# Kernel optimization log

Measured on AMD Instinct MI355X. Metric: run time of the kernel, lower is better.

## Reference

```python
import jax, jax.numpy as jnp
import numpy as np

D_MODEL = 1024
NUM_HEADS = 16
HEAD_DIM = D_MODEL // NUM_HEADS
THETA = 10000.0


def _rope(x):
    # x: [B, H, S, Dk]; interleaved even/odd rotation as in the torch module
    *_, seq_len, d_k = x.shape
    d = d_k // 2
    inv_freq = 1.0 / (THETA ** (2.0 * jnp.arange(d, dtype=jnp.float32) / d_k))
    pos = jnp.arange(seq_len, dtype=jnp.float32)
    angles = pos[:, None] * inv_freq[None, :]  # [S, d]
    cos = jnp.cos(angles)
    sin = jnp.sin(angles)
    x_even = x[..., 0::2]
    x_odd = x[..., 1::2]
    rot_even = x_even * cos - x_odd * sin
    rot_odd = x_even * sin + x_odd * cos
    return jnp.stack([rot_even, rot_odd], axis=-1).reshape(x.shape)


def setup_inputs() -> dict:
    key = jax.random.key(0)
    ks = jax.random.split(key, 5)
    B, S = 4, 2048
    x = jax.random.normal(ks[0], (B, S, D_MODEL), dtype=jnp.float32)
    q_w = jax.random.uniform(ks[1], (D_MODEL, D_MODEL), dtype=jnp.float32)
    k_w = jax.random.uniform(ks[2], (D_MODEL, D_MODEL), dtype=jnp.float32)
    v_w = jax.random.uniform(ks[3], (D_MODEL, D_MODEL), dtype=jnp.float32)
    o_w = jax.random.uniform(ks[4], (D_MODEL, D_MODEL), dtype=jnp.float32)
    return {"x": x, "q_w": q_w, "k_w": k_w, "v_w": v_w, "o_w": o_w}


def reference(x, q_w, k_w, v_w, o_w):
    B, S, _ = x.shape
    def split_heads(t):
        return t.reshape(B, S, NUM_HEADS, HEAD_DIM).transpose(0, 2, 1, 3)  # [B,H,S,Dk]
    Q = split_heads(x @ q_w.T)
    K = split_heads(x @ k_w.T)
    V = split_heads(x @ v_w.T)
    Q = _rope(Q)
    K = _rope(K)
    scale = 1.0 / jnp.sqrt(jnp.float32(HEAD_DIM))
    scores = jnp.einsum('bhqd,bhkd->bhqk', Q, K) * scale  # [B,H,S,S]
    causal = jnp.tril(jnp.ones((S, S), dtype=bool))
    scores = jnp.where(causal[None, None], scores, -jnp.inf)
    attn = jax.nn.softmax(scores, axis=-1)
    out = jnp.einsum('bhqk,bhkd->bhqd', attn, V)  # [B,H,S,Dk]
    out = out.transpose(0, 2, 1, 3).reshape(B, S, D_MODEL)
    return out @ o_w.T
```

## Files before the change

### kernel.cpp

```cpp
#include <hip/hip_runtime.h>
#include <hip/hip_bf16.h>
#include <cstdint>
#include <cstddef>

#define D_MODEL   1024
#define NUM_HEADS 16
#define HEAD_DIM  64
#define SEQ       2048
#define BATCH     4
#define BH        (BATCH*NUM_HEADS)
#define MROWS     (BATCH*SEQ)

typedef _Float16 half8  __attribute__((ext_vector_type(8)));
typedef _Float16 half4v __attribute__((ext_vector_type(4)));
typedef float    floatx4 __attribute__((ext_vector_type(4)));

__device__ inline void gld_lds16(const void* g, void* l) {
    __builtin_amdgcn_global_load_lds(
        (__attribute__((address_space(1))) void*)g,
        (__attribute__((address_space(3))) void*)l,
        16, 0, 0);
}

__global__ void rope_table(float2* __restrict__ tab) {
    const int i = blockIdx.x * blockDim.x + threadIdx.x;
    const int p = i & 31, s = i >> 5;
    const double inv = pow(10000.0, -(double)p / 32.0);
    const double ang = (double)s * inv;
    tab[i] = make_float2((float)cos(ang), (float)sin(ang));
}

__global__ void f32_to_f16_v4(const float* __restrict__ in,
                              _Float16* __restrict__ out, int n4) {
    int i = blockIdx.x * blockDim.x + threadIdx.x;
    if (i >= n4) return;
    float4 v = ((const float4*)in)[i];
    half4v o = { (_Float16)v.x, (_Float16)v.y, (_Float16)v.z, (_Float16)v.w };
    ((half4v*)out)[i] = o;
}

__global__ void f32_split_f16(const float* __restrict__ in,
                              _Float16* __restrict__ hi,
                              _Float16* __restrict__ lo, int n4) {
    int i = blockIdx.x * blockDim.x + threadIdx.x;
    if (i >= n4) return;
    float4 v = ((const float4*)in)[i];
    half4v h = { (_Float16)v.x, (_Float16)v.y, (_Float16)v.z, (_Float16)v.w };
    half4v l = { (_Float16)(v.x - (float)h.x), (_Float16)(v.y - (float)h.y),
                 (_Float16)(v.z - (float)h.z), (_Float16)(v.w - (float)h.w) };
    ((half4v*)hi)[i] = h;
    ((half4v*)lo)[i] = l;
}

template<int MODE>
__global__ __launch_bounds__(256)
void gemm_bt(const _Float16* __restrict__ A, const _Float16* __restrict__ B,
             void* __restrict__ Cout, int M, int N, int K) {
    __shared__ _Float16 As[128*32];
    __shared__ _Float16 Bs[128*32];

    const int nb = N >> 7;
    const int bx = blockIdx.x % nb;
    const int by = blockIdx.x / nb;
    const int m0 = by << 7, n0 = bx << 7;

    const int t    = threadIdx.x;
    const int w    = t >> 6;
    const int lane = t & 63;
    const int r    = lane & 15;
    const int quad = lane >> 4;
    const int wm   = (w >> 1) << 6;
    const int wn   = (w & 1) << 6;

    const int srow = lane >> 2;
    const int scol = (lane & 3) << 3;

    floatx4 acc[4][4];
    #pragma unroll
    for (int i = 0; i < 4; i++)
        #pragma unroll
        for (int j = 0; j < 4; j++)
            acc[i][j] = (floatx4){0.f, 0.f, 0.f, 0.f};

    for (int k0 = 0; k0 < K; k0 += 32) {
        __syncthreads();
        #pragma unroll
        for (int p = 0; p < 2; ++p) {
            const int rbase = p*64 + w*16;
            gld_lds16(&A[(size_t)(m0 + rbase + srow)*K + k0 + scol], &As[rbase*32]);
            gld_lds16(&B[(size_t)(n0 + rbase + srow)*K + k0 + scol], &Bs[rbase*32]);
        }
        __syncthreads();

        half8 af[4], bf[4];
        #pragma unroll
        for (int i = 0; i < 4; i++)
            af[i] = *(const half8*)&As[(wm + i*16 + r)*32 + quad*8];
        #pragma unroll
        for (int j = 0; j < 4; j++)
            bf[j] = *(const half8*)&Bs[(wn + j*16 + r)*32 + quad*8];

        #pragma unroll
        for (int i = 0; i < 4; i++)
            #pragma unroll
            for (int j = 0; j < 4; j++)
                acc[i][j] = __builtin_amdgcn_mfma_f32_16x16x32_f16(
                                af[i], bf[j], acc[i][j], 0, 0, 0);
    }

    #pragma unroll
    for (int i = 0; i < 4; i++) {
        #pragma unroll
        for (int j = 0; j < 4; j++) {
            #pragma unroll
            for (int v = 0; v < 4; v++) {
                const int m = m0 + wm + i*16 + quad*4 + v;
                const int n = n0 + wn + j*16 + r;
                const float val = acc[i][j][v];
                if (MODE == 0) {
                    ((float*)Cout)[(size_t)m*N + n] = val;
                } else {
                    const int b = m >> 11, s = m & 2047;
                    const int h = n >> 6,  d = n & 63;
                    ((_Float16*)Cout)[((((size_t)b*NUM_HEADS + h)*HEAD_DIM + d) << 11) + s]
                        = (_Float16)val;
                }
            }
        }
    }
}

__global__ __launch_bounds__(256)
void gemm_qk(const _Float16* __restrict__ Ah, const _Float16* __restrict__ Al,
             const _Float16* __restrict__ Bh, const _Float16* __restrict__ Bl,
             _Float16* __restrict__ Chi, _Float16* __restrict__ Clo,
             const float2* __restrict__ tab, int M, int N, int K) {
    __shared__ _Float16 Ash[128*32];
    __shared__ _Float16 Asl[128*32];
    __shared__ _Float16 Bsh[128*32];
    __shared__ _Float16 Bsl[128*32];

    const int nb = N >> 7;
    const int bx = blockIdx.x % nb;
    const int by = blockIdx.x / nb;
    const int m0 = by << 7, n0 = bx << 7;

    const int t    = threadIdx.x;
    const int w    = t >> 6;
    const int lane = t & 63;
    const int r    = lane & 15;
    const int quad = lane >> 4;
    const int wm   = (w >> 1) << 6;
    const int wn   = (w & 1) << 6;

    const int srow = lane >> 2;
    const int scol = (lane & 3) << 3;

    floatx4 acc[4][4];
    #pragma unroll
    for (int i = 0; i < 4; i++)
        #pragma unroll
        for (int j = 0; j < 4; j++)
            acc[i][j] = (floatx4){0.f, 0.f, 0.f, 0.f};

    for (int k0 = 0; k0 < K; k0 += 32) {
        __syncthreads();
        #pragma unroll
        for (int p = 0; p < 2; ++p) {
            const int rbase = p*64 + w*16;
            const size_t ga = (size_t)(m0 + rbase + srow)*K + k0 + scol;
            const size_t gb = (size_t)(n0 + rbase + srow)*K + k0 + scol;
            gld_lds16(&Ah[ga], &Ash[rbase*32]);
            gld_lds16(&Al[ga], &Asl[rbase*32]);
            gld_lds16(&Bh[gb], &Bsh[rbase*32]);
            gld_lds16(&Bl[gb], &Bsl[rbase*32]);
        }
        __syncthreads();

        half8 ah[4], al[4], bh[4], bl[4];
        #pragma unroll
        for (int i = 0; i < 4; i++) {
            ah[i] = *(const half8*)&Ash[(wm + i*16 + r)*32 + quad*8];
            al[i] = *(const half8*)&Asl[(wm + i*16 + r)*32 + quad*8];
        }
        #pragma unroll
        for (int j = 0; j < 4; j++) {
            bh[j] = *(const half8*)&Bsh[(wn + j*16 + r)*32 + quad*8];
            bl[j] = *(const half8*)&Bsl[(wn + j*16 + r)*32 + quad*8];
        }

        #pragma unroll
        for (int i = 0; i < 4; i++)
            #pragma unroll
            for (int j = 0; j < 4; j++) {
                acc[i][j] = __builtin_amdgcn_mfma_f32_16x16x32_f16(
                                ah[i], bh[j], acc[i][j], 0, 0, 0);
                acc[i][j] = __builtin_amdgcn_mfma_f32_16x16x32_f16(
                                ah[i], bl[j], acc[i][j], 0, 0, 0);
                acc[i][j] = __builtin_amdgcn_mfma_f32_16x16x32_f16(
                                al[i], bh[j], acc[i][j], 0, 0, 0);
            }
    }

    #pragma unroll
    for (int i = 0; i < 4; i++) {
        #pragma unroll
        for (int v = 0; v < 4; v++) {
            const int m  = m0 + wm + i*16 + quad*4 + v;
            const int b  = m >> 11;
            const int s_ = m & 2047;
            #pragma unroll
            for (int j = 0; j < 4; j++) {
                const int n = n0 + wn + j*16 + r;
                const int h = n >> 6, d = n & 63;
                const float val = acc[i][j][v];
                const float pv  = __shfl_xor(val, 1);
                const float2 cs = tab[s_*32 + (d >> 1)];
                const float res = (r & 1) ? (pv*cs.y + val*cs.x)
                                          : (val*cs.x - pv*cs.y);
                const size_t idx = ((((size_t)b*NUM_HEADS + h)*SEQ + s_) << 6) + d;
                const _Float16 hv = (_Float16)res;
                Chi[idx] = hv;
                Clo[idx] = (_Float16)(res - (float)hv);
            }
        }
    }
}

#define PSTR 72
__global__ __launch_bounds__(256)
void flash_attn(const _Float16* __restrict__ Qhi, const _Float16* __restrict__ Qlo,
                const _Float16* __restrict__ Khi, const _Float16* __restrict__ Klo,
                const _Float16* __restrict__ Vt,  _Float16* __restrict__ AO) {
    __shared__ _Float16 Ksh0[64*32];
    __shared__ _Float16 Ksh1[64*32];
    __shared__ _Float16 Ksl0[64*32];
    __shared__ _Float16 Ksl1[64*32];
    __shared__ _Float16 Vs0 [64*32];
    __shared__ _Float16 Vs1 [64*32];
    __shared__ _Float16 Pl  [4][16*PSTR];

    const int t    = threadIdx.x;
    const int w    = t >> 6;
    const int lane = t & 63;
    const int r    = lane & 15;
    const int quad = lane >> 4;

    const int bx = blockIdx.x;
    const int bh = bx & 63;
    const int qb = 31 - (bx >> 6);
    const int q0w = qb*64 + w*16;
    const int b  = bh >> 4, h = bh & 15;

    const _Float16* Qh_ = Qhi + (size_t)bh * SEQ * HEAD_DIM;
    const _Float16* Ql_ = Qlo + (size_t)bh * SEQ * HEAD_DIM;
    const _Float16* Khg = Khi + (size_t)bh * SEQ * HEAD_DIM;
    const _Float16* Klg = Klo + (size_t)bh * SEQ * HEAD_DIM;
    const _Float16* Vtg = Vt  + (size_t)bh * HEAD_DIM * SEQ;

    half8 qh[2], ql[2];
    #pragma unroll
    for (int c = 0; c < 2; ++c) {
        qh[c] = *(const half8*)&Qh_[(size_t)(q0w + r)*64 + c*32 + quad*8];
        ql[c] = *(const half8*)&Ql_[(size_t)(q0w + r)*64 + c*32 + quad*8];
    }

    floatx4 ot[4];
    #pragma unroll
    for (int dt = 0; dt < 4; ++dt) ot[dt] = (floatx4){0.f,0.f,0.f,0.f};
    float mi = -1e30f, li = 0.f;

    const int sr = lane >> 2;
    const int sc = (lane & 3) << 3;

    const int niter = qb + 1;
    for (int kt = 0; kt < niter; ++kt) {
        const int k0 = kt << 6;

        __syncthreads();
        {
            const int rb  = w << 4;
            const int row = rb + sr;
            const size_t kr = (size_t)(k0 + row)*64;
            gld_lds16(&Khg[kr +      sc], &Ksh0[rb*32]);
            gld_lds16(&Khg[kr + 32 + sc], &Ksh1[rb*32]);
            gld_lds16(&Klg[kr +      sc], &Ksl0[rb*32]);
            gld_lds16(&Klg[kr + 32 + sc], &Ksl1[rb*32]);
            const size_t vr = (size_t)row*SEQ + k0;
            gld_lds16(&Vtg[vr +      sc], &Vs0[rb*32]);
            gld_lds16(&Vtg[vr + 32 + sc], &Vs1[rb*32]);
        }
        __syncthreads();

        float s[16];
        #pragma unroll
        for (int sub = 0; sub < 4; ++sub) {
            floatx4 a = (floatx4){0.f,0.f,0.f,0.f};
            const int fr = (sub*16 + r)*32 + quad*8;
            const half8 kh0 = *(const half8*)&Ksh0[fr];
            const half8 kh1 = *(const half8*)&Ksh1[fr];
            const half8 kl0 = *(const half8*)&Ksl0[fr];
            const half8 kl1 = *(const half8*)&Ksl1[fr];
            a = __builtin_amdgcn_mfma_f32_16x16x32_f16(kh0, qh[0], a, 0, 0, 0);
            a = __builtin_amdgcn_mfma_f32_16x16x32_f16(kh1, qh[1], a, 0, 0, 0);
            a = __builtin_amdgcn_mfma_f32_16x16x32_f16(kh0, ql[0], a, 0, 0, 0);
            a = __builtin_amdgcn_mfma_f32_16x16x32_f16(kh1, ql[1], a, 0, 0, 0);
            a = __builtin_amdgcn_mfma_f32_16x16x32_f16(kl0, qh[0], a, 0, 0, 0);
            a = __builtin_amdgcn_mfma_f32_16x16x32_f16(kl1, qh[1], a, 0, 0, 0);
            #pragma unroll
            for (int v = 0; v < 4; ++v) s[sub*4 + v] = a[v] * 0.125f;
        }

        if (kt == niter - 1) {
            #pragma unroll
            for (int sub = 0; sub < 4; ++sub)
                #pragma unroll
                for (int v = 0; v < 4; ++v)
                    if (k0 + sub*16 + quad*4 + v > q0w + r)
                        s[sub*4 + v] = -1e30f;
        }

        float tm = s[0];
        #pragma unroll
        for (int i = 1; i < 16; ++i) tm = fmaxf(tm, s[i]);
        tm = fmaxf(tm, __shfl_xor(tm, 16));
        tm = fmaxf(tm, __shfl_xor(tm, 32));
        const float mn = fmaxf(mi, tm);
        const float alpha = __expf(mi - mn);
        mi = mn;
        float rs = 0.f;
        #pragma unroll
        for (int i = 0; i < 16; ++i) { s[i] = __expf(s[i] - mn); rs += s[i]; }
        rs += __shfl_xor(rs, 16);
        rs += __shfl_xor(rs, 32);
        li = li*alpha + rs;
        #pragma unroll
        for (int dt = 0; dt < 4; ++dt)
            #pragma unroll
            for (int v = 0; v < 4; ++v) ot[dt][v] *= alpha;

        #pragma unroll
        for (int sub = 0; sub < 4; ++sub) {
            half4v pk = { (_Float16)s[sub*4+0], (_Float16)s[sub*4+1],
                          (_Float16)s[sub*4+2], (_Float16)s[sub*4+3] };
            *(half4v*)&Pl[w][r*PSTR + sub*16 + quad*4] = pk;
        }

        #pragma unroll
        for (int c = 0; c < 2; ++c) {
            const half8 pf = *(const half8*)&Pl[w][r*PSTR + c*32 + quad*8];
            const _Float16* Vsc = c ? Vs1 : Vs0;
            #pragma unroll
            for (int dt = 0; dt < 4; ++dt) {
                const half8 vf = *(const half8*)&Vsc[(dt*16 + r)*32 + quad*8];
                ot[dt] = __builtin_amdgcn_mfma_f32_16x16x32_f16(vf, pf, ot[dt], 0, 0, 0);
            }
        }
    }

    const float inv = 1.0f / li;
    const int q = q0w + r;
    #pragma unroll
    for (int dt = 0; dt < 4; ++dt) {
        half4v o = { (_Float16)(ot[dt][0]*inv), (_Float16)(ot[dt][1]*inv),
                     (_Float16)(ot[dt][2]*inv), (_Float16)(ot[dt][3]*inv) };
        *(half4v*)&AO[((size_t)(b*SEQ + q))*D_MODEL + h*HEAD_DIM + dt*16 + quad*4] = o;
    }
}

extern "C" void kernel_launch(void* const* d_in, const int* in_sizes, int n_in,
                              void* d_out, int out_size, void* d_ws, size_t ws_size,
                              hipStream_t stream) {
    const float* x  = (const float*)d_in[0];
    const float* qw = (const float*)d_in[1];
    const float* kw = (const float*)d_in[2];
    const float* vw = (const float*)d_in[3];
    const float* ow = (const float*)d_in[4];
    float* out = (float*)d_out;

    _Float16* xh  = (_Float16*)d_ws;
    _Float16* xl  = xh  + (size_t)MROWS * D_MODEL;
    _Float16* qwh = xl  + (size_t)MROWS * D_MODEL;
    _Float16* qwl = qwh + (size_t)D_MODEL * D_MODEL;
    _Float16* kwh = qwl + (size_t)D_MODEL * D_MODEL;
    _Float16* kwl = kwh + (size_t)D_MODEL * D_MODEL;
    _Float16* vwh = kwl + (size_t)D_MODEL * D_MODEL;
    _Float16* owh = vwh + (size_t)D_MODEL * D_MODEL;
    _Float16* Qhi = owh + (size_t)D_MODEL * D_MODEL;
    _Float16* Qlo = Qhi + (size_t)MROWS * D_MODEL;
    _Float16* Khi = Qlo + (size_t)MROWS * D_MODEL;
    _Float16* Klo = Khi + (size_t)MROWS * D_MODEL;
    _Float16* Vt  = Klo + (size_t)MROWS * D_MODEL;
    _Float16* AO  = Vt  + (size_t)MROWS * D_MODEL;
    float2*   tab = (float2*)(AO + (size_t)MROWS * D_MODEL);

    rope_table<<<(SEQ*32)/256, 256, 0, stream>>>(tab);

    const int nx4 = MROWS * D_MODEL / 4;
    f32_split_f16<<<nx4/256, 256, 0, stream>>>(x, xh, xl, nx4);
    const int nw4 = D_MODEL * D_MODEL / 4;
    f32_split_f16<<<nw4/256, 256, 0, stream>>>(qw, qwh, qwl, nw4);
    f32_split_f16<<<nw4/256, 256, 0, stream>>>(kw, kwh, kwl, nw4);
    f32_to_f16_v4<<<nw4/256, 256, 0, stream>>>(vw, vwh, nw4);
    f32_to_f16_v4<<<nw4/256, 256, 0, stream>>>(ow, owh, nw4);

    const int gemm_grid = (MROWS/128) * (D_MODEL/128);
    gemm_qk<<<gemm_grid, 256, 0, stream>>>(xh, xl, qwh, qwl, Qhi, Qlo, tab,
                                           MROWS, D_MODEL, D_MODEL);
    gemm_qk<<<gemm_grid, 256, 0, stream>>>(xh, xl, kwh, kwl, Khi, Klo, tab,
                                           MROWS, D_MODEL, D_MODEL);
    gemm_bt<2><<<gemm_grid, 256, 0, stream>>>(xh, vwh, Vt, MROWS, D_MODEL, D_MODEL);

    flash_attn<<<BH * (SEQ/64), 256, 0, stream>>>(Qhi, Qlo, Khi, Klo, Vt, AO);

    gemm_bt<0><<<gemm_grid, 256, 0, stream>>>(AO, owh, out, MROWS, D_MODEL, D_MODEL);
}
```

Measured before the change: 393.4 us.

## Fuse QKV projections into one launch and widen flash-attention blocks to 128 queries

Merges the four weight-conversion launches into one kernel, and merges the Q, K and V projection GEMMs into a single launch whose grid selects the weight matrix per block. Flash attention now runs 512-thread blocks covering 128 queries with 8 waves sharing each K/V tile, so every tile is loaded once for twice as many queries. Waves whose rows lie entirely before a tile skip its compute, and causal masking is applied per wave. This cuts launch count and K/V reload traffic, at the cost of uneven per-wave work inside a block and a larger block that may lower occupancy.

```diff
diff --git a/kernel.cpp b/kernel.cpp
--- a/kernel.cpp
+++ b/kernel.cpp
@@ -28,15 +28,6 @@
     const double inv = pow(10000.0, -(double)p / 32.0);
     const double ang = (double)s * inv;
     tab[i] = make_float2((float)cos(ang), (float)sin(ang));
-}
-
-__global__ void f32_to_f16_v4(const float* __restrict__ in,
-                              _Float16* __restrict__ out, int n4) {
-    int i = blockIdx.x * blockDim.x + threadIdx.x;
-    if (i >= n4) return;
-    float4 v = ((const float4*)in)[i];
-    half4v o = { (_Float16)v.x, (_Float16)v.y, (_Float16)v.z, (_Float16)v.w };
-    ((half4v*)out)[i] = o;
 }
 
 __global__ void f32_split_f16(const float* __restrict__ in,
@@ -52,10 +43,30 @@
     ((half4v*)lo)[i] = l;
 }
 
-template<int MODE>
+__global__ void conv_weights(const float* __restrict__ qw, const float* __restrict__ kw,
+                             const float* __restrict__ vw, const float* __restrict__ ow,
+                             _Float16* __restrict__ qwh, _Float16* __restrict__ qwl,
+                             _Float16* __restrict__ kwh, _Float16* __restrict__ kwl,
+                             _Float16* __restrict__ vwh, _Float16* __restrict__ owh) {
+    const int i = blockIdx.x * blockDim.x + threadIdx.x;
+    const int which = i >> 18;
+    const int j = i & 262143;
+    const float4 v = ((const float4*)(which == 0 ? qw : which == 1 ? kw :
+                                      which == 2 ? vw : ow))[j];
+    half4v h = { (_Float16)v.x, (_Float16)v.y, (_Float16)v.z, (_Float16)v.w };
+    if (which < 2) {
+        half4v l = { (_Float16)(v.x - (float)h.x), (_Float16)(v.y - (float)h.y),
+                     (_Float16)(v.z - (float)h.z), (_Float16)(v.w - (float)h.w) };
+        ((half4v*)(which ? kwh : qwh))[j] = h;
+        ((half4v*)(which ? kwl : qwl))[j] = l;
+    } else {
+        ((half4v*)(which == 2 ? vwh : owh))[j] = h;
+    }
+}
+
 __global__ __launch_bounds__(256)
 void gemm_bt(const _Float16* __restrict__ A, const _Float16* __restrict__ B,
-             void* __restrict__ Cout, int M, int N, int K) {
+             float* __restrict__ Cout, int M, int N, int K) {
     __shared__ _Float16 As[128*32];
     __shared__ _Float16 Bs[128*32];
 
@@ -109,41 +120,39 @@
     }
 
     #pragma unroll
-    for (int i = 0; i < 4; i++) {
-        #pragma unroll
-        for (int j = 0; j < 4; j++) {
+    for (int i = 0; i < 4; i++)
+        #pragma unroll
+        for (int j = 0; j < 4; j++)
             #pragma unroll
             for (int v = 0; v < 4; v++) {
                 const int m = m0 + wm + i*16 + quad*4 + v;
                 const int n = n0 + wn + j*16 + r;
-                const float val = acc[i][j][v];
-                if (MODE == 0) {
-                    ((float*)Cout)[(size_t)m*N + n] = val;
-                } else {
-                    const int b = m >> 11, s = m & 2047;
-                    const int h = n >> 6,  d = n & 63;
-                    ((_Float16*)Cout)[((((size_t)b*NUM_HEADS + h)*HEAD_DIM + d) << 11) + s]
-                        = (_Float16)val;
-                }
-            }
-        }
-    }
+                Cout[(size_t)m*N + n] = acc[i][j][v];
+            }
 }
 
 __global__ __launch_bounds__(256)
-void gemm_qk(const _Float16* __restrict__ Ah, const _Float16* __restrict__ Al,
-             const _Float16* __restrict__ Bh, const _Float16* __restrict__ Bl,
-             _Float16* __restrict__ Chi, _Float16* __restrict__ Clo,
-             const float2* __restrict__ tab, int M, int N, int K) {
+void gemm_qkv(const _Float16* __restrict__ Axh, const _Float16* __restrict__ Axl,
+              const _Float16* __restrict__ qwh, const _Float16* __restrict__ qwl,
+              const _Float16* __restrict__ kwh, const _Float16* __restrict__ kwl,
+              const _Float16* __restrict__ vwh,
+              _Float16* __restrict__ Qhi, _Float16* __restrict__ Qlo,
+              _Float16* __restrict__ Khi, _Float16* __restrict__ Klo,
+              _Float16* __restrict__ Vt,  const float2* __restrict__ tab) {
     __shared__ _Float16 Ash[128*32];
     __shared__ _Float16 Asl[128*32];
     __shared__ _Float16 Bsh[128*32];
     __shared__ _Float16 Bsl[128*32];
 
-    const int nb = N >> 7;
-    const int bx = blockIdx.x % nb;
-    const int by = blockIdx.x / nb;
-    const int m0 = by << 7, n0 = bx << 7;
+    const int bxa = blockIdx.x;
+    const int bx  = bxa % 24;
+    const int by  = bxa / 24;
+    const int wt  = bx >> 3;
+    const int n0  = (bx & 7) << 7;
+    const int m0  = by << 7;
+
+    const _Float16* Bh = (wt == 0) ? qwh : (wt == 1) ? kwh : vwh;
+    const _Float16* Bl = (wt == 0) ? qwl : kwl;
 
     const int t    = threadIdx.x;
     const int w    = t >> 6;
@@ -163,72 +172,107 @@
         for (int j = 0; j < 4; j++)
             acc[i][j] = (floatx4){0.f, 0.f, 0.f, 0.f};
 
-    for (int k0 = 0; k0 < K; k0 += 32) {
+    for (int k0 = 0; k0 < 1024; k0 += 32) {
         __syncthreads();
         #pragma unroll
         for (int p = 0; p < 2; ++p) {
             const int rbase = p*64 + w*16;
-            const size_t ga = (size_t)(m0 + rbase + srow)*K + k0 + scol;
-            const size_t gb = (size_t)(n0 + rbase + srow)*K + k0 + scol;
-            gld_lds16(&Ah[ga], &Ash[rbase*32]);
-            gld_lds16(&Al[ga], &Asl[rbase*32]);
-            gld_lds16(&Bh[gb], &Bsh[rbase*32]);
-            gld_lds16(&Bl[gb], &Bsl[rbase*32]);
-        }
-        __syncthreads();
-
-        half8 ah[4], al[4], bh[4], bl[4];
+            const size_t ga = (size_t)(m0 + rbase + srow)*1024 + k0 + scol;
+            const size_t gb = (size_t)(n0 + rbase + srow)*1024 + k0 + scol;
+            gld_lds16(&Axh[ga], &Ash[rbase*32]);
+            gld_lds16(&Bh [gb], &Bsh[rbase*32]);
+            if (wt < 2) {
+                gld_lds16(&Axl[ga], &Asl[rbase*32]);
+                gld_lds16(&Bl [gb], &Bsl[rbase*32]);
+            }
+        }
+        __syncthreads();
+
+        half8 ah[4], bh[4];
+        #pragma unroll
+        for (int i = 0; i < 4; i++)
+            ah[i] = *(const half8*)&Ash[(wm + i*16 + r)*32 + quad*8];
+        #pragma unroll
+        for (int j = 0; j < 4; j++)
+            bh[j] = *(const half8*)&Bsh[(wn + j*16 + r)*32 + quad*8];
+
+        if (wt < 2) {
+            half8 al[4], bl[4];
+            #pragma unroll
+            for (int i = 0; i < 4; i++)
+                al[i] = *(const half8*)&Asl[(wm + i*16 + r)*32 + quad*8];
+            #pragma unroll
+            for (int j = 0; j < 4; j++)
+                bl[j] = *(const half8*)&Bsl[(wn + j*16 + r)*32 + quad*8];
+            #pragma unroll
+            for (int i = 0; i < 4; i++)
+                #pragma unroll
+                for (int j = 0; j < 4; j++) {
+                    acc[i][j] = __builtin_amdgcn_mfma_f32_16x16x32_f16(
+                                    ah[i], bh[j], acc[i][j], 0, 0, 0);
+                    acc[i][j] = __builtin_amdgcn_mfma_f32_16x16x32_f16(
+                                    ah[i], bl[j], acc[i][j], 0, 0, 0);
+                    acc[i][j] = __builtin_amdgcn_mfma_f32_16x16x32_f16(
+                                    al[i], bh[j], acc[i][j], 0, 0, 0);
+                }
+        } else {
+            #pragma unroll
+            for (int i = 0; i < 4; i++)
+                #pragma unroll
+                for (int j = 0; j < 4; j++)
+                    acc[i][j] = __builtin_amdgcn_mfma_f32_16x16x32_f16(
+                                    ah[i], bh[j], acc[i][j], 0, 0, 0);
+        }
+    }
+
+    if (wt < 2) {
+        _Float16* Chi = wt ? Khi : Qhi;
+        _Float16* Clo = wt ? Klo : Qlo;
         #pragma unroll
         for (int i = 0; i < 4; i++) {
-            ah[i] = *(const half8*)&Ash[(wm + i*16 + r)*32 + quad*8];
-            al[i] = *(const half8*)&Asl[(wm + i*16 + r)*32 + quad*8];
-        }
-        #pragma unroll
-        for (int j = 0; j < 4; j++) {
-            bh[j] = *(const half8*)&Bsh[(wn + j*16 + r)*32 + quad*8];
-            bl[j] = *(const half8*)&Bsl[(wn + j*16 + r)*32 + quad*8];
-        }
-
-        #pragma unroll
-        for (int i = 0; i < 4; i++)
-            #pragma unroll
-            for (int j = 0; j < 4; j++) {
-                acc[i][j] = __builtin_amdgcn_mfma_f32_16x16x32_f16(
-                                ah[i], bh[j], acc[i][j], 0, 0, 0);
-                acc[i][j] = __builtin_amdgcn_mfma_f32_16x16x32_f16(
-                                ah[i], bl[j], acc[i][j], 0, 0, 0);
-                acc[i][j] = __builtin_amdgcn_mfma_f32_16x16x32_f16(
-                                al[i], bh[j], acc[i][j], 0, 0, 0);
-            }
-    }
-
-    #pragma unroll
-    for (int i = 0; i < 4; i++) {
-        #pragma unroll
-        for (int v = 0; v < 4; v++) {
-            const int m  = m0 + wm + i*16 + quad*4 + v;
-            const int b  = m >> 11;
-            const int s_ = m & 2047;
-            #pragma unroll
-            for (int j = 0; j < 4; j++) {
-                const int n = n0 + wn + j*16 + r;
-                const int h = n >> 6, d = n & 63;
-                const float val = acc[i][j][v];
-                const float pv  = __shfl_xor(val, 1);
-                const float2 cs = tab[s_*32 + (d >> 1)];
-                const float res = (r & 1) ? (pv*cs.y + val*cs.x)
-                                          : (val*cs.x - pv*cs.y);
-                const size_t idx = ((((size_t)b*NUM_HEADS + h)*SEQ + s_) << 6) + d;
-                const _Float16 hv = (_Float16)res;
-                Chi[idx] = hv;
-                Clo[idx] = (_Float16)(res - (float)hv);
+            #pragma unroll
+            for (int v = 0; v < 4; v++) {
+                const int m  = m0 + wm + i*16 + quad*4 + v;
+                const int b  = m >> 11;
+                const int s_ = m & 2047;
+                #pragma unroll
+                for (int j = 0; j < 4; j++) {
+                    const int n = n0 + wn + j*16 + r;
+                    const int h = n >> 6, d = n & 63;
+                    const float val = acc[i][j][v];
+                    const float pv  = __shfl_xor(val, 1);
+                    const float2 cs = tab[s_*32 + (d >> 1)];
+                    const float res = (r & 1) ? (pv*cs.y + val*cs.x)
+                                              : (val*cs.x - pv*cs.y);
+                    const size_t idx = ((((size_t)b*NUM_HEADS + h)*SEQ + s_) << 6) + d;
+                    const _Float16 hv = (_Float16)res;
+                    Chi[idx] = hv;
+                    Clo[idx] = (_Float16)(res - (float)hv);
+                }
+            }
+        }
+    } else {
+        #pragma unroll
+        for (int i = 0; i < 4; i++) {
+            #pragma unroll
+            for (int v = 0; v < 4; v++) {
+                const int m  = m0 + wm + i*16 + quad*4 + v;
+                const int b  = m >> 11;
+                const int s_ = m & 2047;
+                #pragma unroll
+                for (int j = 0; j < 4; j++) {
+                    const int n = n0 + wn + j*16 + r;
+                    const int h = n >> 6, d = n & 63;
+                    Vt[((((size_t)b*NUM_HEADS + h)*HEAD_DIM + d) << 11) + s_]
+                        = (_Float16)acc[i][j][v];
+                }
             }
         }
     }
 }
 
 #define PSTR 72
-__global__ __launch_bounds__(256)
+__global__ __launch_bounds__(512)
 void flash_attn(const _Float16* __restrict__ Qhi, const _Float16* __restrict__ Qlo,
                 const _Float16* __restrict__ Khi, const _Float16* __restrict__ Klo,
                 const _Float16* __restrict__ Vt,  _Float16* __restrict__ AO) {
@@ -238,7 +282,7 @@
     __shared__ _Float16 Ksl1[64*32];
     __shared__ _Float16 Vs0 [64*32];
     __shared__ _Float16 Vs1 [64*32];
-    __shared__ _Float16 Pl  [4][16*PSTR];
+    __shared__ _Float16 Pl  [8][16*PSTR];
 
     const int t    = threadIdx.x;
     const int w    = t >> 6;
@@ -248,8 +292,8 @@
 
     const int bx = blockIdx.x;
     const int bh = bx & 63;
-    const int qb = 31 - (bx >> 6);
-    const int q0w = qb*64 + w*16;
+    const int qb = 15 - (bx >> 6);
+    const int q0w = qb*128 + w*16;
     const int b  = bh >> 4, h = bh & 15;
 
     const _Float16* Qh_ = Qhi + (size_t)bh * SEQ * HEAD_DIM;
@@ -273,24 +317,29 @@
     const int sr = lane >> 2;
     const int sc = (lane & 3) << 3;
 
-    const int niter = qb + 1;
+    const int niter = 2*qb + 2;
     for (int kt = 0; kt < niter; ++kt) {
         const int k0 = kt << 6;
 
         __syncthreads();
-        {
-            const int rb  = w << 4;
-            const int row = rb + sr;
-            const size_t kr = (size_t)(k0 + row)*64;
-            gld_lds16(&Khg[kr +      sc], &Ksh0[rb*32]);
-            gld_lds16(&Khg[kr + 32 + sc], &Ksh1[rb*32]);
-            gld_lds16(&Klg[kr +      sc], &Ksl0[rb*32]);
-            gld_lds16(&Klg[kr + 32 + sc], &Ksl1[rb*32]);
-            const size_t vr = (size_t)row*SEQ + k0;
-            gld_lds16(&Vtg[vr +      sc], &Vs0[rb*32]);
-            gld_lds16(&Vtg[vr + 32 + sc], &Vs1[rb*32]);
-        }
-        __syncthreads();
+        #pragma unroll
+        for (int i = 0; i < 3; ++i) {
+            const int strip = w + (i << 3);
+            const int plane = strip >> 2;
+            const int rb    = (strip & 3) << 4;
+            const int row   = rb + sr;
+            switch (plane) {
+            case 0: gld_lds16(&Khg[(size_t)(k0 + row)*64 +      sc], &Ksh0[rb*32]); break;
+            case 1: gld_lds16(&Khg[(size_t)(k0 + row)*64 + 32 + sc], &Ksh1[rb*32]); break;
+            case 2: gld_lds16(&Klg[(size_t)(k0 + row)*64 +      sc], &Ksl0[rb*32]); break;
+            case 3: gld_lds16(&Klg[(size_t)(k0 + row)*64 + 32 + sc], &Ksl1[rb*32]); break;
+            case 4: gld_lds16(&Vtg[(size_t)row*SEQ + k0 +       sc], &Vs0 [rb*32]); break;
+            case 5: gld_lds16(&Vtg[(size_t)row*SEQ + k0 + 32 +  sc], &Vs1 [rb*32]); break;
+            }
+        }
+        __syncthreads();
+
+        if (k0 > q0w + 15) continue;
 
         float s[16];
         #pragma unroll
@@ -311,7 +360,7 @@
             for (int v = 0; v < 4; ++v) s[sub*4 + v] = a[v] * 0.125f;
         }
 
-        if (kt == niter - 1) {
+        if (k0 + 63 > q0w) {
             #pragma unroll
             for (int sub = 0; sub < 4; ++sub)
                 #pragma unroll
@@ -398,20 +447,14 @@
 
     const int nx4 = MROWS * D_MODEL / 4;
     f32_split_f16<<<nx4/256, 256, 0, stream>>>(x, xh, xl, nx4);
-    const int nw4 = D_MODEL * D_MODEL / 4;
-    f32_split_f16<<<nw4/256, 256, 0, stream>>>(qw, qwh, qwl, nw4);
-    f32_split_f16<<<nw4/256, 256, 0, stream>>>(kw, kwh, kwl, nw4);
-    f32_to_f16_v4<<<nw4/256, 256, 0, stream>>>(vw, vwh, nw4);
-    f32_to_f16_v4<<<nw4/256, 256, 0, stream>>>(ow, owh, nw4);
-
-    const int gemm_grid = (MROWS/128) * (D_MODEL/128);
-    gemm_qk<<<gemm_grid, 256, 0, stream>>>(xh, xl, qwh, qwl, Qhi, Qlo, tab,
-                                           MROWS, D_MODEL, D_MODEL);
-    gemm_qk<<<gemm_grid, 256, 0, stream>>>(xh, xl, kwh, kwl, Khi, Klo, tab,
-                                           MROWS, D_MODEL, D_MODEL);
-    gemm_bt<2><<<gemm_grid, 256, 0, stream>>>(xh, vwh, Vt, MROWS, D_MODEL, D_MODEL);
-
-    flash_attn<<<BH * (SEQ/64), 256, 0, stream>>>(Qhi, Qlo, Khi, Klo, Vt, AO);
-
-    gemm_bt<0><<<gemm_grid, 256, 0, stream>>>(AO, owh, out, MROWS, D_MODEL, D_MODEL);
-}
+    conv_weights<<<(4*262144)/256, 256, 0, stream>>>(qw, kw, vw, ow,
+                                                     qwh, qwl, kwh, kwl, vwh, owh);
+
+    gemm_qkv<<<64*24, 256, 0, stream>>>(xh, xl, qwh, qwl, kwh, kwl, vwh,
+                                        Qhi, Qlo, Khi, Klo, Vt, tab);
+
+    flash_attn<<<BH * (SEQ/128), 512, 0, stream>>>(Qhi, Qlo, Khi, Klo, Vt, AO);
+
+    gemm_bt<<<(MROWS/128)*(D_MODEL/128), 256, 0, stream>>>(AO, owh, out,
+                                                           MROWS, D_MODEL, D_MODEL);
+}
```

Measured after the change: 394.0 us. Within noise of the previous version (+0.1%).
